# Performance work log

Hardware: AMD Instinct MI355X
Metric: run time of the kernel (lower is better)

The kernel has to match this reference:

```python
import jax, jax.numpy as jnp
import numpy as np

HIDDEN = 1152
HEADS = 16
HEAD_DIM = HIDDEN // HEADS

def setup_inputs() -> dict:
    key = jax.random.key(0)
    ks = jax.random.split(key, 7)
    s = 1.0 / np.sqrt(HIDDEN)
    return {
        "x": jax.random.normal(ks[0], (16, 1024, HIDDEN), dtype=jnp.float32),
        "w_qkv": jax.random.normal(ks[1], (3 * HIDDEN, HIDDEN), dtype=jnp.float32) * s,
        "b_qkv": jax.random.normal(ks[2], (3 * HIDDEN,), dtype=jnp.float32) * 0.01,
        "q_gamma": jnp.ones((HEAD_DIM,), dtype=jnp.float32),
        "k_gamma": jnp.ones((HEAD_DIM,), dtype=jnp.float32),
        "w_proj": jax.random.normal(ks[3], (HIDDEN, HIDDEN), dtype=jnp.float32) * s,
        "b_proj": jax.random.normal(ks[4], (HIDDEN,), dtype=jnp.float32) * 0.01,
    }

def _rmsnorm(t, gamma):
    # normalize over last dim (head_dim); torch RMSNorm default eps = finfo(dtype).eps
    eps = jnp.asarray(jnp.finfo(t.dtype).eps, t.dtype)
    ms = jnp.mean(jnp.square(t), axis=-1, keepdims=True)
    return t * jax.lax.rsqrt(ms + eps) * gamma

def reference(x, w_qkv, b_qkv, q_gamma, k_gamma, w_proj, b_proj):
    B, S, H = x.shape
    qkv = x @ w_qkv.T + b_qkv                       # [B,S,3H]
    qkv = qkv.reshape(B, S, 3, HEADS, HEAD_DIM)
    qkv = jnp.transpose(qkv, (2, 0, 3, 1, 4))       # [3,B,nh,S,hd]
    q, k, v = qkv[0], qkv[1], qkv[2]
    q = _rmsnorm(q, q_gamma)
    k = _rmsnorm(k, k_gamma)
    scale = 1.0 / np.sqrt(HEAD_DIM)
    scores = jnp.einsum('bhqd,bhkd->bhqk', q, k) * scale
    probs = jax.nn.softmax(scores, axis=-1)
    out = jnp.einsum('bhqk,bhkd->bhqd', probs, v)   # [B,nh,S,hd]
    out = jnp.transpose(out, (0, 2, 1, 3)).reshape(B, S, H)
    return out @ w_proj.T + b_proj
```

## Files before the change

kernel.cpp:

```cpp
#include <hip/hip_runtime.h>

typedef _Float16 f16;
typedef _Float16 f16x8 __attribute__((ext_vector_type(8)));
typedef _Float16 f16x4 __attribute__((ext_vector_type(4)));
typedef float f32x4 __attribute__((ext_vector_type(4)));

__device__ __forceinline__ void gld16(const void* g, void* l) {
    __builtin_amdgcn_global_load_lds(
        (const __attribute__((address_space(1))) void*)g,
        (__attribute__((address_space(3))) void*)l,
        16, 0, 0);
}

__global__ __launch_bounds__(256) void f32_to_f16_vec(const float* __restrict__ in,
                                                      f16* __restrict__ out, long n4) {
    long i = (long)blockIdx.x * 256 + threadIdx.x;
    if (i < n4) {
        float4 v = ((const float4*)in)[i];
        f16x4 o = {(f16)v.x, (f16)v.y, (f16)v.z, (f16)v.w};
        ((f16x4*)out)[i] = o;
    }
}

__global__ __launch_bounds__(256) void gemm_bt(const f16* __restrict__ A,
                                               const f16* __restrict__ B,
                                               const float* __restrict__ bias,
                                               float* __restrict__ Cf,
                                               f16* __restrict__ Ch,
                                               int M, int N, int K) {
    constexpr int BK = 32;
    __shared__ f16 As[128 * BK];
    __shared__ f16 Bs[128 * BK];
    const int tid = threadIdx.x;
    const int w = tid >> 6;
    const int lane = tid & 63;
    const int quad = lane >> 4;
    const int l16 = lane & 15;

    const int nblk = N >> 7;
    const int mblk = M >> 7;
    const int id = blockIdx.x;
    const int xcd = id & 7;
    const int s = id >> 3;
    const int per_band = nblk * 8;
    const int t = s / per_band;
    const int r0 = s - t * per_band;
    const int n_blk = r0 >> 3;
    const int mr = r0 & 7;
    const int bands_per_xcd = mblk >> 6;
    const int m_blk = (xcd * bands_per_xcd + t) * 8 + mr;

    const long m0 = (long)m_blk * 128;
    const long n0 = (long)n_blk * 128;

    const int srow = lane >> 2;
    const int scol = (lane & 3) * 8;
    const f16* gA = A + (m0 + w * 32 + srow) * (long)K + scol;
    const f16* gB = B + (n0 + w * 32 + srow) * (long)K + scol;
    const int lb0 = __builtin_amdgcn_readfirstlane(w * 1024);
    const int lb1 = __builtin_amdgcn_readfirstlane(w * 1024 + 512);

    const int mw = (w >> 1) * 64;
    const int nw = (w & 1) * 64;

    f32x4 acc[4][4] = {};

    for (int k0 = 0; k0 < K; k0 += BK) {
        gld16(gA + k0, &As[lb0]);
        gld16(gA + (long)16 * K + k0, &As[lb1]);
        gld16(gB + k0, &Bs[lb0]);
        gld16(gB + (long)16 * K + k0, &Bs[lb1]);
        __syncthreads();
        f16x8 af[4], bf[4];
#pragma unroll
        for (int t2 = 0; t2 < 4; ++t2)
            af[t2] = *(const f16x8*)&As[(mw + t2 * 16 + l16) * BK + quad * 8];
#pragma unroll
        for (int t2 = 0; t2 < 4; ++t2)
            bf[t2] = *(const f16x8*)&Bs[(nw + t2 * 16 + l16) * BK + quad * 8];
#pragma unroll
        for (int mt = 0; mt < 4; ++mt)
#pragma unroll
            for (int nt = 0; nt < 4; ++nt)
                acc[mt][nt] = __builtin_amdgcn_mfma_f32_16x16x32_f16(
                    af[mt], bf[nt], acc[mt][nt], 0, 0, 0);
        __syncthreads();
    }

    float bv[4];
#pragma unroll
    for (int nt = 0; nt < 4; ++nt)
        bv[nt] = bias ? bias[n0 + nw + nt * 16 + l16] : 0.f;
#pragma unroll
    for (int mt = 0; mt < 4; ++mt) {
#pragma unroll
        for (int r = 0; r < 4; ++r) {
            const long row = m0 + mw + mt * 16 + quad * 4 + r;
#pragma unroll
            for (int nt = 0; nt < 4; ++nt) {
                const long col = n0 + nw + nt * 16 + l16;
                const float v = acc[mt][nt][r] + bv[nt];
                if (Ch) Ch[row * (long)N + col] = (f16)v;
                else    Cf[row * (long)N + col] = v;
            }
        }
    }
}

__global__ __launch_bounds__(256) void qk_norm2(f16* __restrict__ qkv,
                                                const float* __restrict__ qg,
                                                const float* __restrict__ kg,
                                                f16* __restrict__ kc) {
    const float QSCALE = 0.117851130198f;
    const int t = blockIdx.x * 256 + threadIdx.x;
    const int h = t & 15;
    const long bs = t >> 4;
    f16* qp = qkv + bs * 3456 + h * 72;
    {
        f16x8 v[9];
        float ss = 0.f;
#pragma unroll
        for (int c = 0; c < 9; ++c) {
            v[c] = *(const f16x8*)(qp + c * 8);
#pragma unroll
            for (int j = 0; j < 8; ++j) { float f = (float)v[c][j]; ss += f * f; }
        }
        const float rs = rsqrtf(ss * (1.f / 72.f) + 1.1920928955078125e-7f) * QSCALE;
#pragma unroll
        for (int c = 0; c < 9; ++c) {
            f16x8 o;
#pragma unroll
            for (int j = 0; j < 8; ++j) o[j] = (f16)((float)v[c][j] * rs * qg[c * 8 + j]);
            *(f16x8*)(qp + c * 8) = o;
        }
    }
    {
        const f16* kp = qp + 1152;
        f16* dst = kc + ((long)((bs >> 10) * 16 + h) * 1024 + (bs & 1023)) * 72;
        f16x8 v[9];
        float ss = 0.f;
#pragma unroll
        for (int c = 0; c < 9; ++c) {
            v[c] = *(const f16x8*)(kp + c * 8);
#pragma unroll
            for (int j = 0; j < 8; ++j) { float f = (float)v[c][j]; ss += f * f; }
        }
        const float rs = rsqrtf(ss * (1.f / 72.f) + 1.1920928955078125e-7f);
#pragma unroll
        for (int c = 0; c < 9; ++c) {
            f16x8 o;
#pragma unroll
            for (int j = 0; j < 8; ++j) o[j] = (f16)((float)v[c][j] * rs * kg[c * 8 + j]);
            *(f16x8*)(dst + c * 8) = o;
        }
    }
}

__global__ __launch_bounds__(256) void vt_kernel(const f16* __restrict__ QKV,
                                                 f16* __restrict__ Vt) {
    __shared__ f16 tile[64][73];
    const int tid = threadIdx.x;
    const int bh = blockIdx.x;
    const int b = bh >> 4, h = bh & 15;
    const int s0 = blockIdx.y * 64;
    for (int idx = tid; idx < 64 * 72; idx += 256) {
        const int r = idx / 72, c = idx % 72;
        tile[r][c] = QKV[((long)(b * 1024 + s0 + r)) * 3456 + 2304 + h * 72 + c];
    }
    __syncthreads();
    for (int idx = tid; idx < 72 * 64; idx += 256) {
        const int d = idx >> 6, s = idx & 63;
        Vt[((long)bh * 72 + d) * 1024 + s0 + s] = tile[s][d];
    }
}

__global__ __launch_bounds__(256) void attn2(const f16* __restrict__ QKV,
                                             const f16* __restrict__ Kc,
                                             const f16* __restrict__ Vt,
                                             f16* __restrict__ O) {
    constexpr int S = 1024;
    __shared__ f16 smem[64 * 72 + 80 * 76];
    f16* Ks = smem;
    f16* Vs = smem + 64 * 72;
    const int tid = threadIdx.x;
    const int w = tid >> 6, lane = tid & 63;
    const int quad = lane >> 4, l16 = lane & 15;

    const int b = blockIdx.x;
    const int xcd = b & 7;
    const int j = b >> 3;
    const int bh = ((j >> 3) << 3) | xcd;
    const int qt = j & 7;
    const int bb = bh >> 4, h = bh & 15;
    const int q0 = qt * 128;

    for (int i = tid; i < 8 * 76; i += 256) {
        const int pr = i / 76, pc = i % 76;
        Vs[(72 + pr) * 76 + pc] = (pr == 0 && pc < 64) ? (f16)1.f : (f16)0.f;
    }

    const f16* qrow0 = QKV + ((long)(bb * 1024 + q0 + w * 32 + l16)) * 3456 + h * 72;
    const f16* qrow1 = qrow0 + (long)16 * 3456;
    f16x8 qz = {};
    f16x8 qf[2][3];
    qf[0][0] = *(const f16x8*)(qrow0 + quad * 8);
    qf[0][1] = *(const f16x8*)(qrow0 + 32 + quad * 8);
    qf[0][2] = (quad == 0) ? *(const f16x8*)(qrow0 + 64) : qz;
    qf[1][0] = *(const f16x8*)(qrow1 + quad * 8);
    qf[1][1] = *(const f16x8*)(qrow1 + 32 + quad * 8);
    qf[1][2] = (quad == 0) ? *(const f16x8*)(qrow1 + 64) : qz;

    f32x4 o[2][5] = {};

    const f16* gK = Kc + (long)bh * S * 72;
    const f16* gV = Vt + (long)bh * 72 * S;

    for (int s0 = 0; s0 < S; s0 += 64) {
        for (int ch = w; ch < 9; ch += 4)
            gld16(gK + (long)s0 * 72 + ch * 512 + lane * 8,
                  &Ks[__builtin_amdgcn_readfirstlane(ch * 512)]);
#pragma unroll
        for (int it = 0; it < 3; ++it) {
            const int idx = it * 256 + tid;
            if (idx < 576) {
                const int d = idx >> 3, s8 = (idx & 7) * 8;
                f16x8 v = *(const f16x8*)(gV + (long)d * 1024 + s0 + s8);
                f16x4 lo = {v[0], v[1], v[2], v[3]};
                f16x4 hi = {v[4], v[5], v[6], v[7]};
                *(f16x4*)&Vs[d * 76 + s8] = lo;
                *(f16x4*)&Vs[d * 76 + s8 + 4] = hi;
            }
        }
        __syncthreads();

        f32x4 sc[4][2] = {};
#pragma unroll
        for (int ss = 0; ss < 4; ++ss) {
            const int base = (ss * 16 + l16) * 72;
            f16x8 k0 = *(const f16x8*)&Ks[base + quad * 8];
            f16x8 k1 = *(const f16x8*)&Ks[base + 32 + quad * 8];
            f16x8 k2 = *(const f16x8*)&Ks[base + 64 + quad * 8];
            sc[ss][0] = __builtin_amdgcn_mfma_f32_16x16x32_f16(k0, qf[0][0], sc[ss][0], 0, 0, 0);
            sc[ss][0] = __builtin_amdgcn_mfma_f32_16x16x32_f16(k1, qf[0][1], sc[ss][0], 0, 0, 0);
            sc[ss][0] = __builtin_amdgcn_mfma_f32_16x16x32_f16(k2, qf[0][2], sc[ss][0], 0, 0, 0);
            sc[ss][1] = __builtin_amdgcn_mfma_f32_16x16x32_f16(k0, qf[1][0], sc[ss][1], 0, 0, 0);
            sc[ss][1] = __builtin_amdgcn_mfma_f32_16x16x32_f16(k1, qf[1][1], sc[ss][1], 0, 0, 0);
            sc[ss][1] = __builtin_amdgcn_mfma_f32_16x16x32_f16(k2, qf[1][2], sc[ss][1], 0, 0, 0);
        }

        f16x4 pf[4][2];
#pragma unroll
        for (int ss = 0; ss < 4; ++ss)
#pragma unroll
            for (int qs = 0; qs < 2; ++qs) {
                f16x4 pk;
#pragma unroll
                for (int r = 0; r < 4; ++r) pk[r] = (f16)__expf(sc[ss][qs][r]);
                pf[ss][qs] = pk;
            }

#pragma unroll
        for (int vt = 0; vt < 5; ++vt) {
#pragma unroll
            for (int ss = 0; ss < 4; ++ss) {
                f16x4 vf = *(const f16x4*)&Vs[(vt * 16 + l16) * 76 + ss * 16 + quad * 4];
                o[0][vt] = __builtin_amdgcn_mfma_f32_16x16x16f16(vf, pf[ss][0], o[0][vt], 0, 0, 0);
                o[1][vt] = __builtin_amdgcn_mfma_f32_16x16x16f16(vf, pf[ss][1], o[1][vt], 0, 0, 0);
            }
        }
        __syncthreads();
    }

    const float l0 = __shfl(o[0][4][0], 32 + l16);
    const float l1 = __shfl(o[1][4][0], 32 + l16);
    const float inv[2] = {1.f / l0, 1.f / l1};

    f16* es = smem + w * 2560;
#pragma unroll
    for (int qs = 0; qs < 2; ++qs) {
        f16* row = es + (qs * 16 + l16) * 80;
#pragma unroll
        for (int vt = 0; vt < 5; ++vt)
#pragma unroll
            for (int r = 0; r < 4; ++r) {
                const int d = vt * 16 + quad * 4 + r;
                if (d < 72) row[d] = (f16)(o[qs][vt][r] * inv[qs]);
            }
    }
    const long rowbase = (long)bb * 1024 + q0 + w * 32;
#pragma unroll
    for (int it = 0; it < 5; ++it) {
        const int idx = it * 64 + lane;
        if (idx < 288) {
            const int q = idx / 9, c = idx - q * 9;
            f16x4 a = *(const f16x4*)&es[q * 80 + c * 8];
            f16x4 b2 = *(const f16x4*)&es[q * 80 + c * 8 + 4];
            f16* dst = O + (rowbase + q) * 1152 + h * 72 + c * 8;
            *(f16x4*)dst = a;
            *(f16x4*)(dst + 4) = b2;
        }
    }
}

extern "C" void kernel_launch(void* const* d_in, const int* in_sizes, int n_in,
                              void* d_out, int out_size, void* d_ws, size_t ws_size,
                              hipStream_t stream) {
    const float* x       = (const float*)d_in[0];
    const float* w_qkv   = (const float*)d_in[1];
    const float* b_qkv   = (const float*)d_in[2];
    const float* q_gamma = (const float*)d_in[3];
    const float* k_gamma = (const float*)d_in[4];
    const float* w_proj  = (const float*)d_in[5];
    const float* b_proj  = (const float*)d_in[6];
    float* out = (float*)d_out;

    char* p = (char*)d_ws;
    f16* x_h = (f16*)p;      p += (size_t)16384 * 1152 * 2;
    f16* wqkv_h = (f16*)p;   p += (size_t)3456 * 1152 * 2;
    f16* wproj_h = (f16*)p;  p += (size_t)1152 * 1152 * 2;
    f16* qkv_h = (f16*)p;    p += (size_t)16384 * 3456 * 2;
    const size_t needed = (size_t)(p - (char*)d_ws);
    if (ws_size < needed) return;

    f16* k_c = (f16*)d_out;
    f16* v_t = (f16*)d_out + (size_t)16384 * 1152;

    f32_to_f16_vec<<<18432, 256, 0, stream>>>(x, x_h, 16384L * 1152 / 4);
    f32_to_f16_vec<<<3888, 256, 0, stream>>>(w_qkv, wqkv_h, 3456L * 1152 / 4);
    f32_to_f16_vec<<<1296, 256, 0, stream>>>(w_proj, wproj_h, 1152L * 1152 / 4);

    gemm_bt<<<27 * 128, 256, 0, stream>>>(
        x_h, wqkv_h, b_qkv, nullptr, qkv_h, 16384, 3456, 1152);

    qk_norm2<<<1024, 256, 0, stream>>>(qkv_h, q_gamma, k_gamma, k_c);
    vt_kernel<<<dim3(256, 16), 256, 0, stream>>>(qkv_h, v_t);

    attn2<<<2048, 256, 0, stream>>>(qkv_h, k_c, v_t, x_h );

    gemm_bt<<<9 * 128, 256, 0, stream>>>(
        x_h, wproj_h, b_proj, out, nullptr, 16384, 1152, 1152);
}
```

Before: 572.5 us.

## Replace GEMM with 8-wave 256x128 tile kernel using 4-stage LDS pipeline

Replaces the single-buffered 128x128 GEMM with an 8-wave kernel that computes 256x128 tiles, cycling through four LDS buffers so global-to-LDS loads for future K-steps overlap MFMA work. LDS layout is XOR-swizzled to cut bank conflicts, and MFMA phases are interleaved with explicit barriers, waitcnts and setprio. The aim is to hide memory latency and raise tensor-core utilisation in both projection GEMMs. The cost is larger LDS use per block (96KB), hard-coded K (1152) and M-band assumptions, and more intricate synchronisation.

```diff
diff --git a/kernel.cpp b/kernel.cpp
--- a/kernel.cpp
+++ b/kernel.cpp
@@ -22,83 +22,135 @@
     }
 }
 
-__global__ __launch_bounds__(256) void gemm_bt(const f16* __restrict__ A,
-                                               const f16* __restrict__ B,
-                                               const float* __restrict__ bias,
-                                               float* __restrict__ Cf,
-                                               f16* __restrict__ Ch,
-                                               int M, int N, int K) {
-    constexpr int BK = 32;
-    __shared__ f16 As[128 * BK];
-    __shared__ f16 Bs[128 * BK];
+constexpr int GEMM_BUF_E = 12288;
+
+template<int BUF, bool STG>
+__device__ __forceinline__ void tile_step(f16* sm,
+                                          const f16*& pA0, const f16*& pA1,
+                                          const f16*& pB0,
+                                          int dA0, int dA1, int dB0,
+                                          int offA, int offB,
+                                          f32x4 (&acc)[4][4]) {
+    const f16* bp = sm + BUF * GEMM_BUF_E;
+    f16x8 bf[4], af[2];
+#pragma unroll
+    for (int nt = 0; nt < 4; ++nt) bf[nt] = *(const f16x8*)(bp + offB + nt * 512);
+#pragma unroll
+    for (int mt = 0; mt < 2; ++mt) af[mt] = *(const f16x8*)(bp + offA + mt * 512);
+    if (STG) {
+        constexpr int SB = (BUF + 3) & 3;
+        gld16(pA0, sm + SB * GEMM_BUF_E + dA0);
+        gld16(pA1, sm + SB * GEMM_BUF_E + dA1);
+    }
+    __builtin_amdgcn_s_barrier();
+    asm volatile("s_waitcnt lgkmcnt(0)" ::: "memory");
+    __builtin_amdgcn_sched_barrier(0);
+    __builtin_amdgcn_s_setprio(1);
+#pragma unroll
+    for (int mt = 0; mt < 2; ++mt)
+#pragma unroll
+        for (int nt = 0; nt < 4; ++nt)
+            acc[mt][nt] = __builtin_amdgcn_mfma_f32_16x16x32_f16(
+                af[mt], bf[nt], acc[mt][nt], 0, 0, 0);
+    __builtin_amdgcn_s_setprio(0);
+    __builtin_amdgcn_s_barrier();
+    f16x8 ag[2];
+#pragma unroll
+    for (int mt = 0; mt < 2; ++mt) ag[mt] = *(const f16x8*)(bp + offA + 1024 + mt * 512);
+    if (STG) {
+        constexpr int SB = (BUF + 3) & 3;
+        gld16(pB0, sm + SB * GEMM_BUF_E + dB0);
+        pA0 += 32; pA1 += 32; pB0 += 32;
+    }
+    __builtin_amdgcn_s_barrier();
+    asm volatile("s_waitcnt lgkmcnt(0)" ::: "memory");
+    __builtin_amdgcn_sched_barrier(0);
+    __builtin_amdgcn_s_setprio(1);
+#pragma unroll
+    for (int mt = 0; mt < 2; ++mt)
+#pragma unroll
+        for (int nt = 0; nt < 4; ++nt)
+            acc[2 + mt][nt] = __builtin_amdgcn_mfma_f32_16x16x32_f16(
+                ag[mt], bf[nt], acc[2 + mt][nt], 0, 0, 0);
+    __builtin_amdgcn_s_setprio(0);
+}
+
+__global__ __launch_bounds__(512, 2) void gemm8(const f16* __restrict__ A,
+                                                const f16* __restrict__ B,
+                                                const float* __restrict__ bias,
+                                                float* __restrict__ Cf,
+                                                f16* __restrict__ Ch,
+                                                int M, int N, int K) {
+    __shared__ f16 sm[4 * GEMM_BUF_E];
     const int tid = threadIdx.x;
-    const int w = tid >> 6;
-    const int lane = tid & 63;
-    const int quad = lane >> 4;
-    const int l16 = lane & 15;
-
-    const int nblk = N >> 7;
-    const int mblk = M >> 7;
-    const int id = blockIdx.x;
-    const int xcd = id & 7;
-    const int s = id >> 3;
-    const int per_band = nblk * 8;
-    const int t = s / per_band;
-    const int r0 = s - t * per_band;
-    const int n_blk = r0 >> 3;
-    const int mr = r0 & 7;
-    const int bands_per_xcd = mblk >> 6;
-    const int m_blk = (xcd * bands_per_xcd + t) * 8 + mr;
-
-    const long m0 = (long)m_blk * 128;
-    const long n0 = (long)n_blk * 128;
-
-    const int srow = lane >> 2;
-    const int scol = (lane & 3) * 8;
-    const f16* gA = A + (m0 + w * 32 + srow) * (long)K + scol;
-    const f16* gB = B + (n0 + w * 32 + srow) * (long)K + scol;
-    const int lb0 = __builtin_amdgcn_readfirstlane(w * 1024);
-    const int lb1 = __builtin_amdgcn_readfirstlane(w * 1024 + 512);
-
-    const int mw = (w >> 1) * 64;
-    const int nw = (w & 1) * 64;
+    const int w = tid >> 6, lane = tid & 63;
+    const int quad = lane >> 4, l16 = lane & 15;
+    const int wm = w >> 1, wn = w & 1;
+
+    const int nnb = N >> 7;
+    const int mpx = (M >> 8) >> 3;
+    const int xcd = blockIdx.x & 7;
+    const int s = blockIdx.x >> 3;
+    const int mband = s / nnb;
+    const int nblk = s - mband * nnb;
+    const long m0 = (long)(xcd * mpx + mband) << 8;
+    const long n0 = (long)nblk << 7;
+
+    const int r4 = lane >> 2;
+    const int sc = ((lane & 3) ^ ((lane >> 3) & 3)) << 3;
+    const f16* gA0 = A + (m0 + w * 32 + r4) * (long)K + sc;
+    const f16* gA1 = gA0 + (long)16 * K;
+    const f16* gB0 = B + (n0 + w * 16 + r4) * (long)K + sc;
+    const int dA0 = __builtin_amdgcn_readfirstlane(w * 1024);
+    const int dA1 = dA0 + 512;
+    const int dB0 = __builtin_amdgcn_readfirstlane(8192 + w * 512);
+
+    const int swz = (quad ^ ((l16 >> 1) & 3)) << 3;
+    const int offA = (wm * 64 + l16) * 32 + swz;
+    const int offB = 8192 + (wn * 64 + l16) * 32 + swz;
 
     f32x4 acc[4][4] = {};
 
-    for (int k0 = 0; k0 < K; k0 += BK) {
-        gld16(gA + k0, &As[lb0]);
-        gld16(gA + (long)16 * K + k0, &As[lb1]);
-        gld16(gB + k0, &Bs[lb0]);
-        gld16(gB + (long)16 * K + k0, &Bs[lb1]);
-        __syncthreads();
-        f16x8 af[4], bf[4];
-#pragma unroll
-        for (int t2 = 0; t2 < 4; ++t2)
-            af[t2] = *(const f16x8*)&As[(mw + t2 * 16 + l16) * BK + quad * 8];
-#pragma unroll
-        for (int t2 = 0; t2 < 4; ++t2)
-            bf[t2] = *(const f16x8*)&Bs[(nw + t2 * 16 + l16) * BK + quad * 8];
-#pragma unroll
-        for (int mt = 0; mt < 4; ++mt)
-#pragma unroll
-            for (int nt = 0; nt < 4; ++nt)
-                acc[mt][nt] = __builtin_amdgcn_mfma_f32_16x16x32_f16(
-                    af[mt], bf[nt], acc[mt][nt], 0, 0, 0);
-        __syncthreads();
-    }
+#pragma unroll
+    for (int tt = 0; tt < 3; ++tt) {
+        gld16(gA0 + tt * 32, sm + tt * GEMM_BUF_E + dA0);
+        gld16(gA1 + tt * 32, sm + tt * GEMM_BUF_E + dA1);
+        gld16(gB0 + tt * 32, sm + tt * GEMM_BUF_E + dB0);
+    }
+    const f16* pA0 = gA0 + 96;
+    const f16* pA1 = gA1 + 96;
+    const f16* pB0 = gB0 + 96;
+    asm volatile("s_waitcnt vmcnt(6)" ::: "memory");
+    __builtin_amdgcn_s_barrier();
+
+#define VMB(NSTR) asm volatile("s_waitcnt vmcnt(" NSTR ")" ::: "memory"); \
+                  __builtin_amdgcn_s_barrier();
+
+#pragma unroll 1
+    for (int it = 0; it < 8; ++it) {
+        tile_step<0, true>(sm, pA0, pA1, pB0, dA0, dA1, dB0, offA, offB, acc); VMB("6")
+        tile_step<1, true>(sm, pA0, pA1, pB0, dA0, dA1, dB0, offA, offB, acc); VMB("6")
+        tile_step<2, true>(sm, pA0, pA1, pB0, dA0, dA1, dB0, offA, offB, acc); VMB("6")
+        tile_step<3, true>(sm, pA0, pA1, pB0, dA0, dA1, dB0, offA, offB, acc); VMB("6")
+    }
+    tile_step<0, true >(sm, pA0, pA1, pB0, dA0, dA1, dB0, offA, offB, acc); VMB("6")
+    tile_step<1, false>(sm, pA0, pA1, pB0, dA0, dA1, dB0, offA, offB, acc); VMB("3")
+    tile_step<2, false>(sm, pA0, pA1, pB0, dA0, dA1, dB0, offA, offB, acc); VMB("0")
+    tile_step<3, false>(sm, pA0, pA1, pB0, dA0, dA1, dB0, offA, offB, acc);
+#undef VMB
 
     float bv[4];
 #pragma unroll
     for (int nt = 0; nt < 4; ++nt)
-        bv[nt] = bias ? bias[n0 + nw + nt * 16 + l16] : 0.f;
+        bv[nt] = bias ? bias[n0 + wn * 64 + nt * 16 + l16] : 0.f;
 #pragma unroll
     for (int mt = 0; mt < 4; ++mt) {
 #pragma unroll
         for (int r = 0; r < 4; ++r) {
-            const long row = m0 + mw + mt * 16 + quad * 4 + r;
+            const long row = m0 + wm * 64 + mt * 16 + quad * 4 + r;
 #pragma unroll
             for (int nt = 0; nt < 4; ++nt) {
-                const long col = n0 + nw + nt * 16 + l16;
+                const long col = n0 + wn * 64 + nt * 16 + l16;
                 const float v = acc[mt][nt][r] + bv[nt];
                 if (Ch) Ch[row * (long)N + col] = (f16)v;
                 else    Cf[row * (long)N + col] = v;
@@ -329,7 +381,7 @@
     f32_to_f16_vec<<<3888, 256, 0, stream>>>(w_qkv, wqkv_h, 3456L * 1152 / 4);
     f32_to_f16_vec<<<1296, 256, 0, stream>>>(w_proj, wproj_h, 1152L * 1152 / 4);
 
-    gemm_bt<<<27 * 128, 256, 0, stream>>>(
+    gemm8<<<1728, 512, 0, stream>>>(
         x_h, wqkv_h, b_qkv, nullptr, qkv_h, 16384, 3456, 1152);
 
     qk_norm2<<<1024, 256, 0, stream>>>(qkv_h, q_gamma, k_gamma, k_c);
@@ -337,6 +389,6 @@
 
     attn2<<<2048, 256, 0, stream>>>(qkv_h, k_c, v_t, x_h );
 
-    gemm_bt<<<9 * 128, 256, 0, stream>>>(
+    gemm8<<<576, 512, 0, stream>>>(
         x_h, wproj_h, b_proj, out, nullptr, 16384, 1152, 1152);
 }
```

After: 554.4 us. 1.03x faster.
